# Kernel tuning notes

Hardware: AMD Instinct MI355X
Metric: run time of the kernel (lower is better)

The kernel has to match this reference:

```python
import jax, jax.numpy as jnp
import numpy as np

T, H, I, E, K = 4096, 1024, 2048, 32, 4


def setup_inputs() -> dict:
    key = jax.random.key(0)
    ks = jax.random.split(key, 8)
    s = lambda k, shape, std: (jax.random.normal(k, shape, jnp.float32) * std)
    return {
        "x": s(ks[0], (T, H), 1.0),
        "router_w": s(ks[1], (E, H), 0.02),
        "gate_w": s(ks[2], (E, H, I), 0.02),
        "up_w": s(ks[3], (E, H, I), 0.02),
        "down_w": s(ks[4], (E, I, H), 0.02),
        "shared_gate_w": s(ks[5], (H, I), 0.02),
        "shared_up_w": s(ks[6], (H, I), 0.02),
        "shared_down_w": s(ks[7], (I, H), 0.02),
        "top_k": K,
    }


def _moe_forward(x, router_w, gate_w, up_w, down_w, sg, su, sd, top_k):
    # x: [T, H]; expert weights: gate/up [E, H, I], down [E, I, H]
    Tn = x.shape[0]
    En = router_w.shape[0]

    # Router: softmax over experts, top-k selection, renormalize selected probs
    logits = x @ router_w.T                                   # [T, E]
    probs = jax.nn.softmax(logits, axis=-1)
    topk_p, topk_i = jax.lax.top_k(probs, top_k)              # [T, K]
    topk_p = topk_p / jnp.sum(topk_p, axis=-1, keepdims=True)

    # Dense combine weights: combine[t, e] = routing weight of expert e for token t
    combine = jnp.zeros((Tn, En), x.dtype).at[
        jnp.arange(Tn)[:, None], topk_i].add(topk_p)          # [T, E]

    def expert_step(acc, inp):
        wg, wu, wd, c = inp                                   # [H,I], [H,I], [I,H], [T]
        h = jax.nn.silu(x @ wg) * (x @ wu)                    # [T, I] SwiGLU
        return acc + c[:, None] * (h @ wd), None

    acc0 = jnp.zeros_like(x)
    out, _ = jax.lax.scan(expert_step, acc0,
                          (gate_w, up_w, down_w, combine.T))

    # Shared expert: always applied
    shared = (jax.nn.silu(x @ sg) * (x @ su)) @ sd            # [T, H]
    return out + shared


def reference(x, router_w, gate_w, up_w, down_w,
              shared_gate_w, shared_up_w, shared_down_w, top_k):
    return _moe_forward(x, router_w, gate_w, up_w, down_w,
                        shared_gate_w, shared_up_w, shared_down_w, top_k)
```

## Files before the change

kernel.cpp:

```cpp
#include <hip/hip_runtime.h>
#include <hip/hip_bf16.h>

#define T_TOK 4096
#define H_DIM 1024
#define I_DIM 2048
#define N_EXP 32
#define TOPK  4
#define TKTOT (T_TOK * TOPK)
#define ROWS_MAX 24576
#define MAX_TILES 192
#define BM 128
#define BK 64
#define LDB 72

typedef _Float16 f16;
typedef __attribute__((ext_vector_type(2))) f16  f16x2;
typedef __attribute__((ext_vector_type(4))) f16  f16x4;
typedef __attribute__((ext_vector_type(8))) f16  f16x8;
typedef __attribute__((ext_vector_type(4))) float f32x4;

__device__ __forceinline__ void glds16(const f16* g, f16* l) {
  __builtin_amdgcn_global_load_lds(
      (const __attribute__((address_space(1))) void*)g,
      (__attribute__((address_space(3))) void*)l, 16, 0, 0);
}

__global__ void prep_kernel(const float* __restrict__ x, f16* __restrict__ xb,
                            int* __restrict__ row_token,
                            int* __restrict__ counts) {
  int gid = blockIdx.x * blockDim.x + threadIdx.x;
  float4 v = *(const float4*)(x + (size_t)gid * 4);
  f16x4 hv = { (f16)v.x, (f16)v.y, (f16)v.z, (f16)v.w };
  *(f16x4*)(xb + (size_t)gid * 4) = hv;
  if (gid < ROWS_MAX) row_token[gid] = (gid < T_TOK) ? gid : 0;
  if (gid < N_EXP) counts[gid] = 0;
}

__global__ void router_kernel(const float* __restrict__ x,
                              const float* __restrict__ rw,
                              int* __restrict__ expert_sel,
                              float* __restrict__ weight_sel,
                              int* __restrict__ counts) {
  int wid = threadIdx.x >> 6, lane = threadIdx.x & 63;
  int t = blockIdx.x * 4 + wid;
  float xr[16];
#pragma unroll
  for (int j = 0; j < 16; ++j) xr[j] = x[(size_t)t * H_DIM + lane + j * 64];
  float l[32];
#pragma unroll
  for (int e = 0; e < 32; ++e) {
    float p = 0.f;
#pragma unroll
    for (int j = 0; j < 16; ++j) p += xr[j] * rw[(size_t)e * H_DIM + lane + j * 64];
#pragma unroll
    for (int off = 32; off; off >>= 1) p += __shfl_xor(p, off, 64);
    l[e] = p;
  }
  if (lane == 0) {
    unsigned used = 0;
    int sel[4]; float lv[4];
#pragma unroll
    for (int k = 0; k < 4; ++k) {
      float bv = -3.4e38f; int bi = 0;
#pragma unroll
      for (int e = 0; e < 32; ++e) {
        bool better = (((used >> e) & 1u) == 0u) && (l[e] > bv);
        bv = better ? l[e] : bv;
        bi = better ? e : bi;
      }
      used |= 1u << bi; sel[k] = bi; lv[k] = bv;
    }
    float m = lv[0];
    float p0 = __expf(lv[0] - m), p1 = __expf(lv[1] - m);
    float p2 = __expf(lv[2] - m), p3 = __expf(lv[3] - m);
    float s = p0 + p1 + p2 + p3;
    float wv[4] = { p0 / s, p1 / s, p2 / s, p3 / s };
#pragma unroll
    for (int k = 0; k < 4; ++k) {
      expert_sel[t * 4 + k] = sel[k];
      weight_sel[t * 4 + k] = wv[k];
      atomicAdd(&counts[sel[k]], 1);
    }
  }
}

__global__ void scan_kernel(const int* __restrict__ counts, int* __restrict__ cursor,
                            int* __restrict__ tile_expert, int* __restrict__ tile_row0,
                            int* __restrict__ ntiles) {
  if (threadIdx.x != 0 || blockIdx.x != 0) return;
  int nt = 0;
  for (int i = 0; i < T_TOK / BM; ++i) { tile_expert[nt] = N_EXP; tile_row0[nt] = i * BM; ++nt; }
  int pos = T_TOK;
  for (int e = 0; e < N_EXP; ++e) {
    cursor[e] = pos;
    int c = counts[e];
    int nte = (c + BM - 1) / BM;
    for (int i = 0; i < nte; ++i) { tile_expert[nt] = e; tile_row0[nt] = pos + i * BM; ++nt; }
    pos += nte * BM;
  }
  ntiles[0] = nt;
}

__global__ void scatter_kernel(const int* __restrict__ expert_sel,
                               const float* __restrict__ weight_sel,
                               int* __restrict__ cursor,
                               int* __restrict__ row_token,
                               int* __restrict__ slot_of) {
  int i = blockIdx.x * blockDim.x + threadIdx.x;
  if (i >= TKTOT) return;
  int e = expert_sel[i];
  int pos = atomicAdd(&cursor[e], 1);
  row_token[pos] = i >> 2;
  slot_of[i] = pos;
  (void)weight_sel;
}

struct Bf2 { float2 g[8]; };
__device__ __forceinline__ Bf2 fetch_b2(const float* __restrict__ src, size_t ldn) {
  Bf2 r;
#pragma unroll
  for (int j = 0; j < 8; ++j) r.g[j] = *(const float2*)(src + (size_t)j * ldn);
  return r;
}
__device__ __forceinline__ void write_b2(const Bf2& b,
                                         f16 (*__restrict__ Bs)[LDB], int nq, int kr) {
  const float* ga = (const float*)b.g;
  int ks = (8 * kr) ^ ((nq & 7) << 3);
#pragma unroll
  for (int i = 0; i < 2; ++i) {
    union { f16x2 p[4]; f16x8 v; } u;
#pragma unroll
    for (int j = 0; j < 4; ++j)
      u.p[j] = __builtin_bit_cast(
          f16x2, __builtin_amdgcn_cvt_pkrtz(ga[(2 * j) * 2 + i],
                                            ga[(2 * j + 1) * 2 + i]));
    *(f16x8*)&Bs[2 * nq + i][ks] = u.v;
  }
}
__device__ __forceinline__ int rswz1(int row, int kf16) {
  return kf16 ^ (((row >> 1) & 7) << 3);
}

__global__ __launch_bounds__(256, 3) void gemm1_kernel(
    const f16* __restrict__ xb,
    const float* __restrict__ gate_w, const float* __restrict__ up_w,
    const float* __restrict__ sgw, const float* __restrict__ suw,
    const int* __restrict__ row_token,
    const int* __restrict__ tile_expert, const int* __restrict__ tile_row0,
    const int* __restrict__ ntiles, f16* __restrict__ hbuf) {
  int d = blockIdx.y * gridDim.x + blockIdx.x;
  int l = (d & 7) * 768 + (d >> 3);
  int bx = l % MAX_TILES;
  int n0 = (l / MAX_TILES) * 64;
  if (bx >= ntiles[0]) return;
  int e = tile_expert[bx];
  int row0 = tile_row0[bx];
  const float* wg = (e < N_EXP) ? gate_w + (size_t)e * H_DIM * I_DIM : sgw;
  const float* wu = (e < N_EXP) ? up_w   + (size_t)e * H_DIM * I_DIM : suw;

  __shared__ __align__(16) f16 smem[2 * BM * BK + 2 * 64 * LDB];
  f16* A0 = smem;
  f16* A1 = smem + BM * BK;
  f16 (*Bg)[LDB] = (f16(*)[LDB])(smem + 2 * BM * BK);
  f16 (*Bu)[LDB] = (f16(*)[LDB])(smem + 2 * BM * BK + 64 * LDB);
  f16 (*Ct)[LDB] = (f16(*)[LDB])smem;

  int tid = threadIdx.x;
  int lane = tid & 63, wid = tid >> 6;
  int wm = wid >> 1, wn = wid & 1;
  int lr = lane & 15, lk = (lane >> 4) * 8;
  int nq = tid & 31, kr = tid >> 5;

  const f16* abase[4];
#pragma unroll
  for (int it = 0; it < 4; ++it) {
    int idx = tid + it * 256;
    int arow = idx >> 3;
    int atok = row_token[row0 + arow];
    abase[it] = xb + (size_t)atok * H_DIM + ((((idx & 7)) ^ (arow & 7)) << 3);
  }
  const float* wgp = wg + (size_t)(8 * kr) * I_DIM + n0 + 2 * nq;
  const float* wup = wu + (size_t)(8 * kr) * I_DIM + n0 + 2 * nq;

  f32x4 accg[4][2], accu[4][2];
#pragma unroll
  for (int m = 0; m < 4; ++m)
#pragma unroll
    for (int n = 0; n < 2; ++n) { accg[m][n] = (f32x4)0.f; accu[m][n] = (f32x4)0.f; }

#pragma unroll
  for (int it = 0; it < 4; ++it)
    glds16(abase[it], A0 + (tid + it * 256) * 8);
  Bf2 pg = fetch_b2(wgp, I_DIM);
  Bf2 pu = fetch_b2(wup, I_DIM);

  for (int ks = 0; ks < H_DIM / BK; ++ks) {
    write_b2(pg, Bg, nq, kr);
    write_b2(pu, Bu, nq, kr);
    if (ks + 1 < H_DIM / BK) {
      int k0n = (ks + 1) * BK;
      f16* ad = ((ks + 1) & 1) ? A1 : A0;
#pragma unroll
      for (int it = 0; it < 4; ++it)
        glds16(abase[it] + k0n, ad + (tid + it * 256) * 8);
      pg = fetch_b2(wgp + (size_t)k0n * I_DIM, I_DIM);
      pu = fetch_b2(wup + (size_t)k0n * I_DIM, I_DIM);
    }
    __syncthreads();
    const f16* As = (ks & 1) ? A1 : A0;
#pragma unroll
    for (int kk = 0; kk < BK; kk += 32) {
      f16x8 a[4], bg[2], bu[2];
#pragma unroll
      for (int m = 0; m < 4; ++m) {
        int ar = wm * 64 + m * 16 + lr;
        int ko = (kk + lk) ^ ((ar & 7) << 3);
        a[m] = *(const f16x8*)(As + ar * BK + ko);
      }
#pragma unroll
      for (int n = 0; n < 2; ++n) {
        int rowb = wn * 32 + n * 16 + lr;
        int ko = rswz1(rowb, kk + lk);
        bg[n] = *(const f16x8*)&Bg[rowb][ko];
        bu[n] = *(const f16x8*)&Bu[rowb][ko];
      }
#pragma unroll
      for (int m = 0; m < 4; ++m)
#pragma unroll
        for (int n = 0; n < 2; ++n) {
          accg[m][n] = __builtin_amdgcn_mfma_f32_16x16x32_f16(a[m], bg[n], accg[m][n], 0, 0, 0);
          accu[m][n] = __builtin_amdgcn_mfma_f32_16x16x32_f16(a[m], bu[n], accu[m][n], 0, 0, 0);
        }
    }
    __syncthreads();
  }
#pragma unroll
  for (int m = 0; m < 4; ++m)
#pragma unroll
    for (int n = 0; n < 2; ++n)
#pragma unroll
      for (int j = 0; j < 4; ++j) {
        float g = accg[m][n][j], u = accu[m][n][j];
        float hv = g / (1.f + __expf(-g)) * u;
        Ct[wm * 64 + m * 16 + (lane >> 4) * 4 + j][wn * 32 + n * 16 + lr] = (f16)hv;
      }
  __syncthreads();
#pragma unroll
  for (int it = 0; it < 4; ++it) {
    int idx = tid + it * 256;
    int r = idx >> 3, g8 = (idx & 7) * 8;
    *(f16x8*)(hbuf + (size_t)(row0 + r) * I_DIM + n0 + g8) = *(const f16x8*)&Ct[r][g8];
  }
}

__global__ __launch_bounds__(256, 3) void gemm2_kernel(
    const f16* __restrict__ hbuf,
    const float* __restrict__ down_w, const float* __restrict__ sdw,
    const int* __restrict__ tile_expert, const int* __restrict__ tile_row0,
    const int* __restrict__ ntiles, f16* __restrict__ ybuf) {
  int d = blockIdx.y * gridDim.x + blockIdx.x;
  int l = (d & 7) * 384 + (d >> 3);
  int bx = l % MAX_TILES;
  int n0 = (l / MAX_TILES) * 64;
  if (bx >= ntiles[0]) return;
  int e = tile_expert[bx];
  int row0 = tile_row0[bx];
  const float* wd = (e < N_EXP) ? down_w + (size_t)e * I_DIM * H_DIM : sdw;

  __shared__ __align__(16) f16 smem[2 * BM * BK + 64 * LDB];
  f16* A0 = smem;
  f16* A1 = smem + BM * BK;
  f16 (*Bd)[LDB] = (f16(*)[LDB])(smem + 2 * BM * BK);
  f16 (*Ct)[LDB] = (f16(*)[LDB])smem;

  int tid = threadIdx.x;
  int lane = tid & 63, wid = tid >> 6;
  int wm = wid >> 1, wn = wid & 1;
  int lr = lane & 15, lk = (lane >> 4) * 8;
  int nq = tid & 31, kr = tid >> 5;

  const f16* abase[4];
#pragma unroll
  for (int it = 0; it < 4; ++it) {
    int idx = tid + it * 256;
    int arow = idx >> 3;
    abase[it] = hbuf + (size_t)(row0 + arow) * I_DIM + ((((idx & 7)) ^ (arow & 7)) << 3);
  }
  const float* wdp = wd + (size_t)(8 * kr) * H_DIM + n0 + 2 * nq;

  f32x4 acc[4][2];
#pragma unroll
  for (int m = 0; m < 4; ++m)
#pragma unroll
    for (int n = 0; n < 2; ++n) acc[m][n] = (f32x4)0.f;

#pragma unroll
  for (int it = 0; it < 4; ++it)
    glds16(abase[it], A0 + (tid + it * 256) * 8);
  Bf2 pd = fetch_b2(wdp, H_DIM);

  for (int ks = 0; ks < I_DIM / BK; ++ks) {
    write_b2(pd, Bd, nq, kr);
    if (ks + 1 < I_DIM / BK) {
      int k0n = (ks + 1) * BK;
      f16* ad = ((ks + 1) & 1) ? A1 : A0;
#pragma unroll
      for (int it = 0; it < 4; ++it)
        glds16(abase[it] + k0n, ad + (tid + it * 256) * 8);
      pd = fetch_b2(wdp + (size_t)k0n * H_DIM, H_DIM);
    }
    __syncthreads();
    const f16* As = (ks & 1) ? A1 : A0;
#pragma unroll
    for (int kk = 0; kk < BK; kk += 32) {
      f16x8 a[4], bd[2];
#pragma unroll
      for (int m = 0; m < 4; ++m) {
        int ar = wm * 64 + m * 16 + lr;
        int ko = (kk + lk) ^ ((ar & 7) << 3);
        a[m] = *(const f16x8*)(As + ar * BK + ko);
      }
#pragma unroll
      for (int n = 0; n < 2; ++n) {
        int rowb = wn * 32 + n * 16 + lr;
        bd[n] = *(const f16x8*)&Bd[rowb][rswz1(rowb, kk + lk)];
      }
#pragma unroll
      for (int m = 0; m < 4; ++m)
#pragma unroll
        for (int n = 0; n < 2; ++n)
          acc[m][n] = __builtin_amdgcn_mfma_f32_16x16x32_f16(a[m], bd[n], acc[m][n], 0, 0, 0);
    }
    __syncthreads();
  }
#pragma unroll
  for (int m = 0; m < 4; ++m)
#pragma unroll
    for (int n = 0; n < 2; ++n)
#pragma unroll
      for (int j = 0; j < 4; ++j)
        Ct[wm * 64 + m * 16 + (lane >> 4) * 4 + j][wn * 32 + n * 16 + lr] =
            (f16)acc[m][n][j];
  __syncthreads();
#pragma unroll
  for (int it = 0; it < 4; ++it) {
    int idx = tid + it * 256;
    int r = idx >> 3, g8 = (idx & 7) * 8;
    *(f16x8*)(ybuf + (size_t)(row0 + r) * H_DIM + n0 + g8) = *(const f16x8*)&Ct[r][g8];
  }
}

__global__ void gather_kernel(const f16* __restrict__ ybuf,
                              const int* __restrict__ slot_of,
                              const float* __restrict__ weight_sel,
                              float* __restrict__ out) {
  int gid = blockIdx.x * blockDim.x + threadIdx.x;
  int t = gid >> 7, s8 = (gid & 127) * 8;
  f16x8 ysh = *(const f16x8*)(ybuf + (size_t)t * H_DIM + s8);
  float a[8];
#pragma unroll
  for (int j = 0; j < 8; ++j) a[j] = (float)ysh[j];
#pragma unroll
  for (int k = 0; k < 4; ++k) {
    int sl = slot_of[t * 4 + k];
    float w = weight_sel[t * 4 + k];
    f16x8 v = *(const f16x8*)(ybuf + (size_t)sl * H_DIM + s8);
#pragma unroll
    for (int j = 0; j < 8; ++j) a[j] += w * (float)v[j];
  }
  float4 o0 = { a[0], a[1], a[2], a[3] };
  float4 o1 = { a[4], a[5], a[6], a[7] };
  *(float4*)(out + (size_t)t * H_DIM + s8) = o0;
  *(float4*)(out + (size_t)t * H_DIM + s8 + 4) = o1;
}

extern "C" void kernel_launch(void* const* d_in, const int* in_sizes, int n_in,
                              void* d_out, int out_size, void* d_ws, size_t ws_size,
                              hipStream_t stream) {
  const float* x        = (const float*)d_in[0];
  const float* router_w = (const float*)d_in[1];
  const float* gate_w   = (const float*)d_in[2];
  const float* up_w     = (const float*)d_in[3];
  const float* down_w   = (const float*)d_in[4];
  const float* sgw      = (const float*)d_in[5];
  const float* suw      = (const float*)d_in[6];
  const float* sdw      = (const float*)d_in[7];
  float* out = (float*)d_out;

  char* w = (char*)d_ws;
  f16*   xb         = (f16*)w;   w += (size_t)T_TOK * H_DIM * 2;
  int*   expert_sel = (int*)w;   w += (size_t)TKTOT * 4;
  float* weight_sel = (float*)w; w += (size_t)TKTOT * 4;
  int*   slot_of    = (int*)w;   w += (size_t)TKTOT * 4;
  int*   counts     = (int*)w;   w += 256;
  int*   cursor     = (int*)w;   w += 256;
  int*   tile_exp   = (int*)w;   w += MAX_TILES * 4;
  int*   tile_row0  = (int*)w;   w += MAX_TILES * 4;
  int*   ntiles     = (int*)w;   w += 256;
  int*   row_token  = (int*)w;   w += (size_t)ROWS_MAX * 4;
  f16*   hbuf       = (f16*)w;   w += (size_t)ROWS_MAX * I_DIM * 2;
  f16*   ybuf       = (f16*)w;   w += (size_t)ROWS_MAX * H_DIM * 2;
  if ((size_t)(w - (char*)d_ws) > ws_size) return;

  prep_kernel<<<(T_TOK * H_DIM / 4) / 256, 256, 0, stream>>>(x, xb, row_token, counts);
  router_kernel<<<T_TOK / 4, 256, 0, stream>>>(x, router_w, expert_sel, weight_sel, counts);
  scan_kernel<<<1, 64, 0, stream>>>(counts, cursor, tile_exp, tile_row0, ntiles);
  scatter_kernel<<<TKTOT / 256, 256, 0, stream>>>(expert_sel, weight_sel, cursor, row_token, slot_of);
  gemm1_kernel<<<dim3(MAX_TILES, I_DIM / 64), 256, 0, stream>>>(
      xb, gate_w, up_w, sgw, suw, row_token, tile_exp, tile_row0, ntiles, hbuf);
  gemm2_kernel<<<dim3(MAX_TILES, H_DIM / 64), 256, 0, stream>>>(
      hbuf, down_w, sdw, tile_exp, tile_row0, ntiles, ybuf);
  gather_kernel<<<(T_TOK * (H_DIM / 8)) / 256, 256, 0, stream>>>(
      ybuf, slot_of, weight_sel, out);
}
```

Baseline: 745.6 us.

## Widen gemm2 N tile to 128 and add scheduling barriers with MFMA priority

The down-projection GEMM tile grows from 128x64 to 128x128: each wave computes 4x4 MFMA blocks, B is fetched as float4, a new swizzle is used, and the grid and remap are adjusted. This halves how often the A (hbuf) tiles are re-read per output column and raises compute per block, at the cost of more accumulator registers and LDS. Both GEMMs also replace __syncthreads with explicit lgkmcnt waits plus s_barrier wrapped in sched_barrier fences, and raise wave priority with s_setprio during the MFMA section so that memory issue and math overlap better. An unused scatter argument is removed.

```diff
diff --git a/kernel.cpp b/kernel.cpp
--- a/kernel.cpp
+++ b/kernel.cpp
@@ -23,6 +23,19 @@
   __builtin_amdgcn_global_load_lds(
       (const __attribute__((address_space(1))) void*)g,
       (__attribute__((address_space(3))) void*)l, 16, 0, 0);
+}
+__device__ __forceinline__ void sfence() { __builtin_amdgcn_sched_barrier(0); }
+__device__ __forceinline__ void bar_pre() {
+  sfence();
+  asm volatile("s_waitcnt lgkmcnt(0)" ::: "memory");
+  sfence();
+  __builtin_amdgcn_s_barrier();
+  sfence();
+}
+__device__ __forceinline__ void bar_post() {
+  sfence();
+  __builtin_amdgcn_s_barrier();
+  sfence();
 }
 
 __global__ void prep_kernel(const float* __restrict__ x, f16* __restrict__ xb,
@@ -102,7 +115,6 @@
 }
 
 __global__ void scatter_kernel(const int* __restrict__ expert_sel,
-                               const float* __restrict__ weight_sel,
                                int* __restrict__ cursor,
                                int* __restrict__ row_token,
                                int* __restrict__ slot_of) {
@@ -112,7 +124,6 @@
   int pos = atomicAdd(&cursor[e], 1);
   row_token[pos] = i >> 2;
   slot_of[i] = pos;
-  (void)weight_sel;
 }
 
 struct Bf2 { float2 g[8]; };
@@ -139,6 +150,32 @@
 }
 __device__ __forceinline__ int rswz1(int row, int kf16) {
   return kf16 ^ (((row >> 1) & 7) << 3);
+}
+
+struct Bf4 { float4 g[8]; };
+__device__ __forceinline__ Bf4 fetch_b4(const float* __restrict__ src, size_t ldn) {
+  Bf4 r;
+#pragma unroll
+  for (int j = 0; j < 8; ++j) r.g[j] = *(const float4*)(src + (size_t)j * ldn);
+  return r;
+}
+__device__ __forceinline__ void write_b4(const Bf4& b,
+                                         f16 (*__restrict__ Bs)[LDB], int nq, int kr) {
+  const float* ga = (const float*)b.g;
+  int ks = (8 * kr) ^ ((nq & 7) << 3);
+#pragma unroll
+  for (int i = 0; i < 4; ++i) {
+    union { f16x2 p[4]; f16x8 v; } u;
+#pragma unroll
+    for (int j = 0; j < 4; ++j)
+      u.p[j] = __builtin_bit_cast(
+          f16x2, __builtin_amdgcn_cvt_pkrtz(ga[(2 * j) * 4 + i],
+                                            ga[(2 * j + 1) * 4 + i]));
+    *(f16x8*)&Bs[4 * nq + i][ks] = u.v;
+  }
+}
+__device__ __forceinline__ int rswz2(int row, int kf16) {
+  return kf16 ^ (((row >> 2) & 7) << 3);
 }
 
 __global__ __launch_bounds__(256, 3) void gemm1_kernel(
@@ -188,26 +225,34 @@
 #pragma unroll
     for (int n = 0; n < 2; ++n) { accg[m][n] = (f32x4)0.f; accu[m][n] = (f32x4)0.f; }
 
+  sfence();
 #pragma unroll
   for (int it = 0; it < 4; ++it)
     glds16(abase[it], A0 + (tid + it * 256) * 8);
+  sfence();
   Bf2 pg = fetch_b2(wgp, I_DIM);
   Bf2 pu = fetch_b2(wup, I_DIM);
-
-  for (int ks = 0; ks < H_DIM / BK; ++ks) {
+  sfence();
+
+  const int NK = H_DIM / BK;
+  for (int ks = 0; ks < NK; ++ks) {
     write_b2(pg, Bg, nq, kr);
     write_b2(pu, Bu, nq, kr);
-    if (ks + 1 < H_DIM / BK) {
+    if (ks + 1 < NK) {
       int k0n = (ks + 1) * BK;
       f16* ad = ((ks + 1) & 1) ? A1 : A0;
+      sfence();
 #pragma unroll
       for (int it = 0; it < 4; ++it)
         glds16(abase[it] + k0n, ad + (tid + it * 256) * 8);
+      sfence();
       pg = fetch_b2(wgp + (size_t)k0n * I_DIM, I_DIM);
       pu = fetch_b2(wup + (size_t)k0n * I_DIM, I_DIM);
-    }
-    __syncthreads();
+      sfence();
+    }
+    bar_pre();
     const f16* As = (ks & 1) ? A1 : A0;
+    __builtin_amdgcn_s_setprio(1);
 #pragma unroll
     for (int kk = 0; kk < BK; kk += 32) {
       f16x8 a[4], bg[2], bu[2];
@@ -232,7 +277,8 @@
           accu[m][n] = __builtin_amdgcn_mfma_f32_16x16x32_f16(a[m], bu[n], accu[m][n], 0, 0, 0);
         }
     }
-    __syncthreads();
+    __builtin_amdgcn_s_setprio(0);
+    bar_post();
   }
 #pragma unroll
   for (int m = 0; m < 4; ++m)
@@ -259,19 +305,19 @@
     const int* __restrict__ tile_expert, const int* __restrict__ tile_row0,
     const int* __restrict__ ntiles, f16* __restrict__ ybuf) {
   int d = blockIdx.y * gridDim.x + blockIdx.x;
-  int l = (d & 7) * 384 + (d >> 3);
+  int l = (d & 7) * 192 + (d >> 3);
   int bx = l % MAX_TILES;
-  int n0 = (l / MAX_TILES) * 64;
+  int n0 = (l / MAX_TILES) * 128;
   if (bx >= ntiles[0]) return;
   int e = tile_expert[bx];
   int row0 = tile_row0[bx];
   const float* wd = (e < N_EXP) ? down_w + (size_t)e * I_DIM * H_DIM : sdw;
 
-  __shared__ __align__(16) f16 smem[2 * BM * BK + 64 * LDB];
+  __shared__ __align__(16) f16 smem[2 * BM * BK + 128 * LDB];
   f16* A0 = smem;
   f16* A1 = smem + BM * BK;
   f16 (*Bd)[LDB] = (f16(*)[LDB])(smem + 2 * BM * BK);
-  f16 (*Ct)[LDB] = (f16(*)[LDB])smem;
+  f16 (*Ct)[136] = (f16(*)[136])smem;
 
   int tid = threadIdx.x;
   int lane = tid & 63, wid = tid >> 6;
@@ -286,34 +332,42 @@
     int arow = idx >> 3;
     abase[it] = hbuf + (size_t)(row0 + arow) * I_DIM + ((((idx & 7)) ^ (arow & 7)) << 3);
   }
-  const float* wdp = wd + (size_t)(8 * kr) * H_DIM + n0 + 2 * nq;
-
-  f32x4 acc[4][2];
+  const float* wdp = wd + (size_t)(8 * kr) * H_DIM + n0 + 4 * nq;
+
+  f32x4 acc[4][4];
 #pragma unroll
   for (int m = 0; m < 4; ++m)
 #pragma unroll
-    for (int n = 0; n < 2; ++n) acc[m][n] = (f32x4)0.f;
-
+    for (int n = 0; n < 4; ++n) acc[m][n] = (f32x4)0.f;
+
+  sfence();
 #pragma unroll
   for (int it = 0; it < 4; ++it)
     glds16(abase[it], A0 + (tid + it * 256) * 8);
-  Bf2 pd = fetch_b2(wdp, H_DIM);
-
-  for (int ks = 0; ks < I_DIM / BK; ++ks) {
-    write_b2(pd, Bd, nq, kr);
-    if (ks + 1 < I_DIM / BK) {
+  sfence();
+  Bf4 pd = fetch_b4(wdp, H_DIM);
+  sfence();
+
+  const int NK = I_DIM / BK;
+  for (int ks = 0; ks < NK; ++ks) {
+    write_b4(pd, Bd, nq, kr);
+    if (ks + 1 < NK) {
       int k0n = (ks + 1) * BK;
       f16* ad = ((ks + 1) & 1) ? A1 : A0;
+      sfence();
 #pragma unroll
       for (int it = 0; it < 4; ++it)
         glds16(abase[it] + k0n, ad + (tid + it * 256) * 8);
-      pd = fetch_b2(wdp + (size_t)k0n * H_DIM, H_DIM);
-    }
-    __syncthreads();
+      sfence();
+      pd = fetch_b4(wdp + (size_t)k0n * H_DIM, H_DIM);
+      sfence();
+    }
+    bar_pre();
     const f16* As = (ks & 1) ? A1 : A0;
+    __builtin_amdgcn_s_setprio(1);
 #pragma unroll
     for (int kk = 0; kk < BK; kk += 32) {
-      f16x8 a[4], bd[2];
+      f16x8 a[4], bd[4];
 #pragma unroll
       for (int m = 0; m < 4; ++m) {
         int ar = wm * 64 + m * 16 + lr;
@@ -321,31 +375,32 @@
         a[m] = *(const f16x8*)(As + ar * BK + ko);
       }
 #pragma unroll
-      for (int n = 0; n < 2; ++n) {
-        int rowb = wn * 32 + n * 16 + lr;
-        bd[n] = *(const f16x8*)&Bd[rowb][rswz1(rowb, kk + lk)];
+      for (int n = 0; n < 4; ++n) {
+        int rowb = wn * 64 + n * 16 + lr;
+        bd[n] = *(const f16x8*)&Bd[rowb][rswz2(rowb, kk + lk)];
       }
 #pragma unroll
       for (int m = 0; m < 4; ++m)
 #pragma unroll
-        for (int n = 0; n < 2; ++n)
+        for (int n = 0; n < 4; ++n)
           acc[m][n] = __builtin_amdgcn_mfma_f32_16x16x32_f16(a[m], bd[n], acc[m][n], 0, 0, 0);
     }
-    __syncthreads();
+    __builtin_amdgcn_s_setprio(0);
+    bar_post();
   }
 #pragma unroll
   for (int m = 0; m < 4; ++m)
 #pragma unroll
-    for (int n = 0; n < 2; ++n)
+    for (int n = 0; n < 4; ++n)
 #pragma unroll
       for (int j = 0; j < 4; ++j)
-        Ct[wm * 64 + m * 16 + (lane >> 4) * 4 + j][wn * 32 + n * 16 + lr] =
+        Ct[wm * 64 + m * 16 + (lane >> 4) * 4 + j][wn * 64 + n * 16 + lr] =
             (f16)acc[m][n][j];
   __syncthreads();
 #pragma unroll
-  for (int it = 0; it < 4; ++it) {
+  for (int it = 0; it < 8; ++it) {
     int idx = tid + it * 256;
-    int r = idx >> 3, g8 = (idx & 7) * 8;
+    int r = idx >> 4, g8 = (idx & 15) * 8;
     *(f16x8*)(ybuf + (size_t)(row0 + r) * H_DIM + n0 + g8) = *(const f16x8*)&Ct[r][g8];
   }
 }
@@ -405,10 +460,10 @@
   prep_kernel<<<(T_TOK * H_DIM / 4) / 256, 256, 0, stream>>>(x, xb, row_token, counts);
   router_kernel<<<T_TOK / 4, 256, 0, stream>>>(x, router_w, expert_sel, weight_sel, counts);
   scan_kernel<<<1, 64, 0, stream>>>(counts, cursor, tile_exp, tile_row0, ntiles);
-  scatter_kernel<<<TKTOT / 256, 256, 0, stream>>>(expert_sel, weight_sel, cursor, row_token, slot_of);
+  scatter_kernel<<<TKTOT / 256, 256, 0, stream>>>(expert_sel, cursor, row_token, slot_of);
   gemm1_kernel<<<dim3(MAX_TILES, I_DIM / 64), 256, 0, stream>>>(
       xb, gate_w, up_w, sgw, suw, row_token, tile_exp, tile_row0, ntiles, hbuf);
-  gemm2_kernel<<<dim3(MAX_TILES, H_DIM / 64), 256, 0, stream>>>(
+  gemm2_kernel<<<dim3(MAX_TILES, H_DIM / 128), 256, 0, stream>>>(
       hbuf, down_w, sdw, tile_exp, tile_row0, ntiles, ybuf);
   gather_kernel<<<(T_TOK * (H_DIM / 8)) / 256, 256, 0, stream>>>(
       ybuf, slot_of, weight_sel, out);
```

After: 653.0 us. -12.4%, faster.
